# Kernel tuning notes

Hardware: AMD Instinct MI355X
Metric: run time of the kernel (lower is better)

Reference implementation:

```python
import jax, jax.numpy as jnp
import numpy as np

EPS = 0.1  # FAConv default eps


def setup_inputs() -> dict:
    key = jax.random.key(0)
    k1, k2, k3, k4, k5 = jax.random.split(key, 5)
    N, D, E, Dout = 50000, 128, 600000, 128
    x = jax.random.normal(k1, (N, D), dtype=jnp.float32)
    edge_index = jax.random.randint(k2, (2, E), 0, N, dtype=jnp.int64)
    # glorot-style scale for att vectors (Linear(D,1)) and weight matrix
    att_l = jax.random.normal(k3, (D,), dtype=jnp.float32) * (1.0 / np.sqrt(D))
    att_r = jax.random.normal(k4, (D,), dtype=jnp.float32) * (1.0 / np.sqrt(D))
    weight = jax.random.normal(k5, (D, Dout), dtype=jnp.float32) * np.sqrt(6.0 / (D + Dout))
    bias = jnp.zeros((Dout,), dtype=jnp.float32)
    return {"x": x, "edge_index": edge_index, "att_l": att_l, "att_r": att_r,
            "weight": weight, "bias": bias}


def reference(x, edge_index, att_l, att_r, weight, bias):
    N, D = x.shape
    # gcn_norm with add_self_loops=True
    loops = jnp.arange(N, dtype=edge_index.dtype)
    row = jnp.concatenate([edge_index[0], loops])  # source nodes
    col = jnp.concatenate([edge_index[1], loops])  # target nodes
    deg = jax.ops.segment_sum(jnp.ones_like(col, dtype=x.dtype), col, num_segments=N)
    dinv = jnp.where(deg > 0, jax.lax.rsqrt(jnp.maximum(deg, 1e-12)), 0.0)
    norm = dinv[row] * dinv[col]  # [E+N]
    # FAConv attention: alpha = tanh(att_l . x_j + att_r . x_i)
    al = x @ att_l  # [N]
    ar = x @ att_r  # [N]
    a = jnp.tanh(al[row] + ar[col])  # per-edge
    msg = x[row] * (a * norm)[:, None]  # [E+N, D]
    agg = jax.ops.segment_sum(msg, col, num_segments=N)
    h = agg + EPS * x  # x_0 == x in SAGNN.forward
    return h @ weight + bias
```

## Files before the change

### kernel.cpp

```cpp
#include <hip/hip_runtime.h>
#include <hip/hip_bf16.h>

#define FA_EPS 0.1f
#define BUCKET_M 48

typedef _Float16 half8  __attribute__((ext_vector_type(8)));
typedef _Float16 half4v __attribute__((ext_vector_type(4)));
typedef float    f32x4  __attribute__((ext_vector_type(4)));

__global__ __launch_bounds__(256) void k_node_prep(
    const float* __restrict__ x,
    const float* __restrict__ att_l,
    const float* __restrict__ att_r,
    const float* __restrict__ w,
    float* __restrict__ al, float* __restrict__ ar,
    _Float16* __restrict__ x16, _Float16* __restrict__ wt, int N)
{
    int gtid = (int)(blockIdx.x * blockDim.x + threadIdx.x);
    if (gtid < 128 * 128) {
        int k = gtid >> 7, n = gtid & 127;
        wt[n * 128 + k] = (_Float16)w[k * 128 + n];
    }
    int wave = gtid >> 6;
    int lane = threadIdx.x & 63;
    int half = lane >> 5;
    int sl   = lane & 31;
    int node = wave * 2 + half;
    if (node >= N) return;
    const float4* xr = (const float4*)(x + (size_t)node * 128);
    float4 v  = xr[sl];
    float4 l4 = ((const float4*)att_l)[sl];
    float4 r4 = ((const float4*)att_r)[sl];
    half4v hv;
    hv[0] = (_Float16)v.x; hv[1] = (_Float16)v.y;
    hv[2] = (_Float16)v.z; hv[3] = (_Float16)v.w;
    *((half4v*)(x16 + (size_t)node * 128) + sl) = hv;
    float pal = v.x * l4.x + v.y * l4.y + v.z * l4.z + v.w * l4.w;
    float par = v.x * r4.x + v.y * r4.y + v.z * r4.z + v.w * r4.w;
    #pragma unroll
    for (int off = 16; off > 0; off >>= 1) {
        pal += __shfl_xor(pal, off);
        par += __shfl_xor(par, off);
    }
    if (sl == 0) {
        al[node] = pal;
        ar[node] = par;
    }
}

__global__ __launch_bounds__(256) void k_edge(
    const int* __restrict__ ei,
    const float* __restrict__ al, const float* __restrict__ ar,
    unsigned int* __restrict__ deg,
    int2* __restrict__ csr, int E)
{
    int e = (int)(blockIdx.x * blockDim.x + threadIdx.x);
    if (e >= E) return;
    int s = ei[e];
    int t = ei[E + e];
    float th = tanhf(al[s] + ar[t]);
    unsigned int pos = atomicAdd(&deg[t], 1u);
    if (pos < BUCKET_M)
        csr[(size_t)t * BUCKET_M + pos] = make_int2(s, __float_as_int(th));
}

__global__ __launch_bounds__(256) void k_gather(
    const _Float16* __restrict__ x16,
    const int2* __restrict__ csr,
    const unsigned int* __restrict__ deg,
    const float* __restrict__ al, const float* __restrict__ ar,
    _Float16* __restrict__ h16, int N)
{
    int wave = (int)((blockIdx.x * blockDim.x + threadIdx.x) >> 6);
    int lane = threadIdx.x & 63;
    int g  = lane >> 4;
    int sl = lane & 15;
    int t  = wave * 4 + g;
    bool valid = t < N;
    int tc = valid ? t : N - 1;
    unsigned int dt = deg[tc];
    unsigned int cnt = dt < BUCKET_M ? dt : BUCKET_M;
    if (!valid) cnt = 0u;
    float dinv_t = rsqrtf((float)(dt + 1u));
    const int2* cs = csr + (size_t)tc * BUCKET_M;
    float acc[8];
    #pragma unroll
    for (int c = 0; c < 8; ++c) acc[c] = 0.f;
    for (unsigned int j = 0; j < cnt; j += 4) {
        int2 e[4];
        #pragma unroll
        for (int u = 0; u < 4; ++u) {
            unsigned int idx = j + u;
            if (idx >= cnt) idx = cnt - 1;
            e[u] = cs[idx];
        }
        #pragma unroll
        for (int u = 0; u < 4; ++u)
            if (j + u >= cnt) e[u].y = 0;
        unsigned int ds[4];
        half8 v[4];
        #pragma unroll
        for (int u = 0; u < 4; ++u) {
            ds[u] = deg[e[u].x];
            v[u]  = *((const half8*)(x16 + (size_t)e[u].x * 128) + sl);
        }
        #pragma unroll
        for (int u = 0; u < 4; ++u) {
            float a = __int_as_float(e[u].y)
                    * rsqrtf((float)(ds[u] + 1u)) * dinv_t;
            #pragma unroll
            for (int c = 0; c < 8; ++c) acc[c] += a * (float)v[u][c];
        }
    }
    float coef = tanhf(al[tc] + ar[tc]) * dinv_t * dinv_t + FA_EPS;
    half8 vt = *((const half8*)(x16 + (size_t)tc * 128) + sl);
    #pragma unroll
    for (int c = 0; c < 8; ++c) acc[c] += coef * (float)vt[c];
    if (valid) {
        half8 hv;
        #pragma unroll
        for (int c = 0; c < 8; ++c) hv[c] = (_Float16)acc[c];
        *((half8*)(h16 + (size_t)t * 128) + sl) = hv;
    }
}

__global__ __launch_bounds__(256) void k_matmul_mfma(
    const _Float16* __restrict__ h16,
    const _Float16* __restrict__ wt,
    const float* __restrict__ bias,
    float* __restrict__ out, int N)
{
    __shared__ _Float16 wl[128 * 136];
    int tid = threadIdx.x;
    {
        const float* wsrc = (const float*)wt;
        float* wdst = (float*)wl;
        #pragma unroll
        for (int i = tid; i < 8192; i += 256)
            wdst[(i >> 6) * 68 + (i & 63)] = wsrc[i];
    }
    __syncthreads();
    int wv   = tid >> 6;
    int lane = tid & 63;
    int m    = lane & 15;
    int quad = lane >> 4;
    int r0 = (int)blockIdx.x * 64 + wv * 16;
    f32x4 acc[8];
    #pragma unroll
    for (int t = 0; t < 8; ++t) acc[t] = (f32x4)0.f;
    const _Float16* arow = h16 + (size_t)(r0 + m) * 128 + quad * 8;
    #pragma unroll
    for (int k0 = 0; k0 < 128; k0 += 32) {
        half8 a = *(const half8*)(arow + k0);
        #pragma unroll
        for (int t = 0; t < 8; ++t) {
            const _Float16* bp = wl + (size_t)(t * 16 + m) * 136 + quad * 8 + k0;
            half8 b = *(const half8*)bp;
            acc[t] = __builtin_amdgcn_mfma_f32_16x16x32_f16(a, b, acc[t], 0, 0, 0);
        }
    }
    int orow = r0 + quad * 4;
    #pragma unroll
    for (int t = 0; t < 8; ++t) {
        int col = t * 16 + m;
        float bc = bias[col];
        #pragma unroll
        for (int rg = 0; rg < 4; ++rg) {
            int r = orow + rg;
            if (r < N) out[(size_t)r * 128 + col] = acc[t][rg] + bc;
        }
    }
}

extern "C" void kernel_launch(void* const* d_in, const int* in_sizes, int n_in,
                              void* d_out, int out_size, void* d_ws, size_t ws_size,
                              hipStream_t stream)
{
    const float* x     = (const float*)d_in[0];
    const int*   ei    = (const int*)d_in[1];
    const float* att_l = (const float*)d_in[2];
    const float* att_r = (const float*)d_in[3];
    const float* w     = (const float*)d_in[4];
    const float* bias  = (const float*)d_in[5];
    float* out = (float*)d_out;

    const int N  = in_sizes[0] / 128;
    const int E  = in_sizes[1] / 2;
    const int NP = ((N + 63) / 64) * 64;

    char* ws = (char*)d_ws;
    _Float16*     h16 = (_Float16*)ws;
    _Float16*     x16 = h16 + (size_t)NP * 128;
    float*        al  = (float*)(x16 + (size_t)N * 128);
    float*        ar  = al + N;
    unsigned int* deg = (unsigned int*)(ar + N);
    int2*         csr = (int2*)(deg + N);
    _Float16*     wt  = (_Float16*)(csr + (size_t)N * BUCKET_M);

    hipMemsetAsync(deg, 0, (size_t)N * sizeof(unsigned int), stream);

    {
        int waves = (N + 1) / 2;
        k_node_prep<<<(waves * 64 + 255) / 256, 256, 0, stream>>>(
            x, att_l, att_r, w, al, ar, x16, wt, N);
    }
    k_edge<<<(E + 255) / 256, 256, 0, stream>>>(ei, al, ar, deg, csr, E);
    {
        int waves = (N + 3) / 4;
        k_gather<<<(waves * 64 + 255) / 256, 256, 0, stream>>>(
            x16, csr, deg, al, ar, h16, N);
    }
    k_matmul_mfma<<<NP / 64, 256, 0, stream>>>(h16, wt, bias, out, N);
}
```

Measured before the change: 162.4 us.

## Pack degree with al, drop memset, compute tanh in gather

Degree and the left attention score are packed into one 8-byte record per node. The degree counter is zeroed inside node prep, which removes the separate memset launch. The edge kernel now only does the atomic and stores the 4-byte source index, so the CSR bucket shrinks by half. The tanh moves to the gather, so one load fetches both degree and al for each source, at the cost of a tanh per edge in the gather's inner loop.

```diff
diff --git a/kernel.cpp b/kernel.cpp
--- a/kernel.cpp
+++ b/kernel.cpp
@@ -7,13 +7,14 @@
 typedef _Float16 half8  __attribute__((ext_vector_type(8)));
 typedef _Float16 half4v __attribute__((ext_vector_type(4)));
 typedef float    f32x4  __attribute__((ext_vector_type(4)));
+
 
 __global__ __launch_bounds__(256) void k_node_prep(
     const float* __restrict__ x,
     const float* __restrict__ att_l,
     const float* __restrict__ att_r,
     const float* __restrict__ w,
-    float* __restrict__ al, float* __restrict__ ar,
+    uint2* __restrict__ R, float* __restrict__ ar,
     _Float16* __restrict__ x16, _Float16* __restrict__ wt, int N)
 {
     int gtid = (int)(blockIdx.x * blockDim.x + threadIdx.x);
@@ -43,32 +44,30 @@
         par += __shfl_xor(par, off);
     }
     if (sl == 0) {
-        al[node] = pal;
+        R[node] = make_uint2(0u, __float_as_uint(pal));
         ar[node] = par;
     }
 }
 
 __global__ __launch_bounds__(256) void k_edge(
     const int* __restrict__ ei,
-    const float* __restrict__ al, const float* __restrict__ ar,
-    unsigned int* __restrict__ deg,
-    int2* __restrict__ csr, int E)
+    uint2* __restrict__ R,
+    unsigned int* __restrict__ csr, int E)
 {
     int e = (int)(blockIdx.x * blockDim.x + threadIdx.x);
     if (e >= E) return;
     int s = ei[e];
     int t = ei[E + e];
-    float th = tanhf(al[s] + ar[t]);
-    unsigned int pos = atomicAdd(&deg[t], 1u);
+    unsigned int pos = atomicAdd((unsigned int*)(R + t), 1u);
     if (pos < BUCKET_M)
-        csr[(size_t)t * BUCKET_M + pos] = make_int2(s, __float_as_int(th));
+        csr[(size_t)t * BUCKET_M + pos] = (unsigned int)s;
 }
 
 __global__ __launch_bounds__(256) void k_gather(
     const _Float16* __restrict__ x16,
-    const int2* __restrict__ csr,
-    const unsigned int* __restrict__ deg,
-    const float* __restrict__ al, const float* __restrict__ ar,
+    const unsigned int* __restrict__ csr,
+    const uint2* __restrict__ R,
+    const float* __restrict__ ar,
     _Float16* __restrict__ h16, int N)
 {
     int wave = (int)((blockIdx.x * blockDim.x + threadIdx.x) >> 6);
@@ -78,41 +77,44 @@
     int t  = wave * 4 + g;
     bool valid = t < N;
     int tc = valid ? t : N - 1;
-    unsigned int dt = deg[tc];
+    uint2 rt = R[tc];
+    unsigned int dt = rt.x;
+    float al_t = __uint_as_float(rt.y);
+    float ar_t = ar[tc];
     unsigned int cnt = dt < BUCKET_M ? dt : BUCKET_M;
     if (!valid) cnt = 0u;
     float dinv_t = rsqrtf((float)(dt + 1u));
-    const int2* cs = csr + (size_t)tc * BUCKET_M;
+    const unsigned int* cs = csr + (size_t)tc * BUCKET_M;
     float acc[8];
     #pragma unroll
     for (int c = 0; c < 8; ++c) acc[c] = 0.f;
     for (unsigned int j = 0; j < cnt; j += 4) {
-        int2 e[4];
+        unsigned int e[4];
+        float msel[4];
         #pragma unroll
         for (int u = 0; u < 4; ++u) {
             unsigned int idx = j + u;
+            msel[u] = (idx < cnt) ? 1.f : 0.f;
             if (idx >= cnt) idx = cnt - 1;
             e[u] = cs[idx];
         }
-        #pragma unroll
-        for (int u = 0; u < 4; ++u)
-            if (j + u >= cnt) e[u].y = 0;
-        unsigned int ds[4];
+        uint2 rs[4];
         half8 v[4];
         #pragma unroll
         for (int u = 0; u < 4; ++u) {
-            ds[u] = deg[e[u].x];
-            v[u]  = *((const half8*)(x16 + (size_t)e[u].x * 128) + sl);
+            rs[u] = R[e[u]];
+            v[u]  = *((const half8*)(x16 + (size_t)e[u] * 128) + sl);
         }
         #pragma unroll
         for (int u = 0; u < 4; ++u) {
-            float a = __int_as_float(e[u].y)
-                    * rsqrtf((float)(ds[u] + 1u)) * dinv_t;
+            float al_s = __uint_as_float(rs[u].y);
+            float a = msel[u] * tanhf(al_s + ar_t)
+                    * rsqrtf((float)(rs[u].x + 1u)) * dinv_t;
             #pragma unroll
             for (int c = 0; c < 8; ++c) acc[c] += a * (float)v[u][c];
         }
     }
-    float coef = tanhf(al[tc] + ar[tc]) * dinv_t * dinv_t + FA_EPS;
+    float coef = tanhf(al_t + ar_t) * dinv_t * dinv_t + FA_EPS;
     half8 vt = *((const half8*)(x16 + (size_t)tc * 128) + sl);
     #pragma unroll
     for (int c = 0; c < 8; ++c) acc[c] += coef * (float)vt[c];
@@ -191,24 +193,21 @@
     char* ws = (char*)d_ws;
     _Float16*     h16 = (_Float16*)ws;
     _Float16*     x16 = h16 + (size_t)NP * 128;
-    float*        al  = (float*)(x16 + (size_t)N * 128);
-    float*        ar  = al + N;
-    unsigned int* deg = (unsigned int*)(ar + N);
-    int2*         csr = (int2*)(deg + N);
+    uint2*        R   = (uint2*)(x16 + (size_t)N * 128);
+    float*        ar  = (float*)(R + N);
+    unsigned int* csr = (unsigned int*)(ar + N);
     _Float16*     wt  = (_Float16*)(csr + (size_t)N * BUCKET_M);
-
-    hipMemsetAsync(deg, 0, (size_t)N * sizeof(unsigned int), stream);
 
     {
         int waves = (N + 1) / 2;
         k_node_prep<<<(waves * 64 + 255) / 256, 256, 0, stream>>>(
-            x, att_l, att_r, w, al, ar, x16, wt, N);
-    }
-    k_edge<<<(E + 255) / 256, 256, 0, stream>>>(ei, al, ar, deg, csr, E);
+            x, att_l, att_r, w, R, ar, x16, wt, N);
+    }
+    k_edge<<<(E + 255) / 256, 256, 0, stream>>>(ei, R, csr, E);
     {
         int waves = (N + 3) / 4;
         k_gather<<<(waves * 64 + 255) / 256, 256, 0, stream>>>(
-            x16, csr, deg, al, ar, h16, N);
+            x16, csr, R, ar, h16, N);
     }
     k_matmul_mfma<<<NP / 64, 256, 0, stream>>>(h16, wt, bias, out, N);
 }
```

Result: faster. 157.2 us (-3.2%).
